# Performance work log

Measured on AMD Instinct MI355X. Metric: run time of the kernel, lower is better.

Reference implementation:

```python
import jax, jax.numpy as jnp
import numpy as np

SEQ, BATCH, EMBED = 2048, 4, 768
NUM_HEADS = 12
HEAD_DIM = EMBED // NUM_HEADS
SCALING = HEAD_DIM ** -0.5


def setup_inputs() -> dict:
    key = jax.random.key(0)
    ks = jax.random.split(key, 9)
    std = 0.02
    d = {"x": jax.random.normal(ks[0], (SEQ, BATCH, EMBED), dtype=jnp.float32)}
    for i, n in enumerate(["q", "k", "v", "out"]):
        d[f"W{n}"] = jax.random.normal(ks[1 + 2 * i], (EMBED, EMBED), dtype=jnp.float32) * std
        d[f"b{n}"] = jax.random.normal(ks[2 + 2 * i], (EMBED,), dtype=jnp.float32) * std
    return d


def reference(x, Wq, bq, Wk, bk, Wv, bv, Wout, bout):
    # x: [tgt_len, bsz, embed_dim] (fairseq seq-first layout per forward body)
    T, B, E = x.shape
    H, Dh = NUM_HEADS, HEAD_DIM

    q = (x @ Wq.T + bq) * SCALING          # [T, B, E]
    k = x @ Wk.T + bk
    v = x @ Wv.T + bv

    # view(T, B*H, Dh).transpose(0, 1) -> [B*H, T, Dh]
    q = q.reshape(T, B * H, Dh).transpose(1, 0, 2)
    k = k.reshape(T, B * H, Dh).transpose(1, 0, 2)
    v = v.reshape(T, B * H, Dh).transpose(1, 0, 2)

    # bmm: [B*H, T, T] attention scores (full O(T^2) matrix, as in the original)
    scores = jnp.einsum('bqd,bkd->bqk', q, k)
    # util_softmax with onnx_trace=True: softmax in float32, then cast back
    probs = jax.nn.softmax(scores.astype(jnp.float32), axis=-1).astype(scores.dtype)
    # dropout p=0.0 -> identity

    attn = jnp.einsum('bqk,bkd->bqd', probs, v)           # [B*H, T, Dh]
    attn = attn.transpose(1, 0, 2).reshape(T, B, E)       # [T, B, E]
    return attn @ Wout.T + bout
```

## Files before the change

kernel.cpp:

```cpp
#include <hip/hip_runtime.h>
#include <hip/hip_bf16.h>

#define SEQ 2048
#define BATCH 4
#define EMBED 768
#define NHEAD 12
#define HDIM 64
#define NROWS (SEQ*BATCH)
#define GH (BATCH*NHEAD)
#define KVBLK 64

typedef __bf16 bf16;
typedef __attribute__((ext_vector_type(4))) __bf16 bf16x4;
typedef __attribute__((ext_vector_type(8))) __bf16 bf16x8;
typedef __attribute__((ext_vector_type(4))) float f32x4;

#define LOG2E 1.44269504088896340736f

__global__ __launch_bounds__(256) void cvt_kernel(const float* __restrict__ in,
                                                  bf16* __restrict__ out, int n4) {
  int i = blockIdx.x * 256 + threadIdx.x;
  if (i >= n4) return;
  float4 v = reinterpret_cast<const float4*>(in)[i];
  bf16x4 o;
  o[0] = (bf16)v.x; o[1] = (bf16)v.y; o[2] = (bf16)v.z; o[3] = (bf16)v.w;
  reinterpret_cast<bf16x4*>(out)[i] = o;
}

__global__ __launch_bounds__(256) void cvt_w4(const float* __restrict__ Wq,
                                              const float* __restrict__ Wk,
                                              const float* __restrict__ Wv,
                                              const float* __restrict__ Wo,
                                              bf16* __restrict__ Wqkvb,
                                              bf16* __restrict__ Wob) {
  const int n4 = EMBED * EMBED / 4;
  int i = blockIdx.x * 256 + threadIdx.x;
  if (i >= n4) return;
  const float* src;
  bf16* dst;
  switch (blockIdx.y) {
    case 0: src = Wq; dst = Wqkvb; break;
    case 1: src = Wk; dst = Wqkvb + EMBED * EMBED; break;
    case 2: src = Wv; dst = Wqkvb + 2 * EMBED * EMBED; break;
    default: src = Wo; dst = Wob; break;
  }
  float4 v = reinterpret_cast<const float4*>(src)[i];
  bf16x4 o;
  o[0] = (bf16)v.x; o[1] = (bf16)v.y; o[2] = (bf16)v.z; o[3] = (bf16)v.w;
  reinterpret_cast<bf16x4*>(dst)[i] = o;
}

__global__ __launch_bounds__(256) void gemm_qkv(const bf16* __restrict__ A,
                                                const bf16* __restrict__ B,
                                                const float* __restrict__ bq,
                                                const float* __restrict__ bk,
                                                const float* __restrict__ bv,
                                                bf16* __restrict__ Qh,
                                                bf16* __restrict__ Kh,
                                                bf16* __restrict__ Vt) {
  constexpr int K = EMBED;
  __shared__ bf16 As[128 * 32];
  __shared__ bf16 Bs[128 * 32];
  const int tid = threadIdx.x;
  const int l = tid & 63;
  const int w = tid >> 6;
  const int row0 = blockIdx.x * 128;
  const int col0 = blockIdx.y * 128;
  const int wm = (w >> 1) * 64;
  const int wn = (w & 1) * 64;
  const int l15 = l & 15, l4 = l >> 4;

  f32x4 acc[4][4] = {};

  for (int k0 = 0; k0 < K; k0 += 32) {
#pragma unroll
    for (int i = 0; i < 2; ++i) {
      int c = tid + i * 256;
      int r = c >> 2, cc = c & 3;
      __builtin_amdgcn_global_load_lds(
          (const __attribute__((address_space(1))) void*)(A + (size_t)(row0 + r) * K + k0 + cc * 8),
          (__attribute__((address_space(3))) void*)(As + c * 8), 16, 0, 0);
    }
#pragma unroll
    for (int i = 0; i < 2; ++i) {
      int c = tid + i * 256;
      int r = c >> 2, cc = c & 3;
      __builtin_amdgcn_global_load_lds(
          (const __attribute__((address_space(1))) void*)(B + (size_t)(col0 + r) * K + k0 + cc * 8),
          (__attribute__((address_space(3))) void*)(Bs + c * 8), 16, 0, 0);
    }
    __syncthreads();

    bf16x8 af[4], bfr[4];
#pragma unroll
    for (int i = 0; i < 4; ++i)
      af[i] = *reinterpret_cast<const bf16x8*>(&As[(wm + i * 16 + l15) * 32 + l4 * 8]);
#pragma unroll
    for (int j = 0; j < 4; ++j)
      bfr[j] = *reinterpret_cast<const bf16x8*>(&Bs[(wn + j * 16 + l15) * 32 + l4 * 8]);
#pragma unroll
    for (int i = 0; i < 4; ++i)
#pragma unroll
      for (int j = 0; j < 4; ++j)
        acc[i][j] = __builtin_amdgcn_mfma_f32_16x16x32_bf16(af[i], bfr[j], acc[i][j], 0, 0, 0);
    __syncthreads();
  }

  const int sel = blockIdx.y / 6;
  const float* bias = sel == 0 ? bq : (sel == 1 ? bk : bv);
  const int colbase = col0 - sel * EMBED;
#pragma unroll
  for (int i = 0; i < 4; ++i) {
#pragma unroll
    for (int j = 0; j < 4; ++j) {
      int col = colbase + wn + j * 16 + l15;
      float bia = bias[col];
#pragma unroll
      for (int r = 0; r < 4; ++r) {
        int row = row0 + wm + i * 16 + l4 * 4 + r;
        float v = acc[i][j][r] + bia;
        int t = row >> 2, bb = row & 3;
        int hh = col >> 6, d = col & 63;
        int g = bb * NHEAD + hh;
        if (sel == 0)      Qh[((size_t)g * SEQ + t) * HDIM + d] = (bf16)(v * (0.125f * LOG2E));
        else if (sel == 1) Kh[((size_t)g * SEQ + t) * HDIM + d] = (bf16)v;
        else               Vt[((size_t)g * HDIM + d) * SEQ + t] = (bf16)v;
      }
    }
  }
}

__global__ __launch_bounds__(256) void gemm_out(const bf16* __restrict__ A,
                                                const bf16* __restrict__ B,
                                                const float* __restrict__ bias,
                                                float* __restrict__ outp) {
  constexpr int K = EMBED;
  __shared__ bf16 As[128 * 32];
  __shared__ bf16 Bs[128 * 32];
  const int tid = threadIdx.x;
  const int l = tid & 63;
  const int w = tid >> 6;
  const int row0 = blockIdx.x * 128;
  const int col0 = blockIdx.y * 128;
  const int wm = (w >> 1) * 64;
  const int wn = (w & 1) * 64;
  const int l15 = l & 15, l4 = l >> 4;

  f32x4 acc[4][4] = {};

  for (int k0 = 0; k0 < K; k0 += 32) {
#pragma unroll
    for (int i = 0; i < 2; ++i) {
      int c = tid + i * 256;
      int r = c >> 2, cc = c & 3;
      __builtin_amdgcn_global_load_lds(
          (const __attribute__((address_space(1))) void*)(A + (size_t)(row0 + r) * K + k0 + cc * 8),
          (__attribute__((address_space(3))) void*)(As + c * 8), 16, 0, 0);
    }
#pragma unroll
    for (int i = 0; i < 2; ++i) {
      int c = tid + i * 256;
      int r = c >> 2, cc = c & 3;
      __builtin_amdgcn_global_load_lds(
          (const __attribute__((address_space(1))) void*)(B + (size_t)(col0 + r) * K + k0 + cc * 8),
          (__attribute__((address_space(3))) void*)(Bs + c * 8), 16, 0, 0);
    }
    __syncthreads();

    bf16x8 af[4], bfr[4];
#pragma unroll
    for (int i = 0; i < 4; ++i)
      af[i] = *reinterpret_cast<const bf16x8*>(&As[(wm + i * 16 + l15) * 32 + l4 * 8]);
#pragma unroll
    for (int j = 0; j < 4; ++j)
      bfr[j] = *reinterpret_cast<const bf16x8*>(&Bs[(wn + j * 16 + l15) * 32 + l4 * 8]);
#pragma unroll
    for (int i = 0; i < 4; ++i)
#pragma unroll
      for (int j = 0; j < 4; ++j)
        acc[i][j] = __builtin_amdgcn_mfma_f32_16x16x32_bf16(af[i], bfr[j], acc[i][j], 0, 0, 0);
    __syncthreads();
  }

#pragma unroll
  for (int i = 0; i < 4; ++i) {
#pragma unroll
    for (int j = 0; j < 4; ++j) {
      int col = col0 + wn + j * 16 + l15;
      float bia = bias[col];
#pragma unroll
      for (int r = 0; r < 4; ++r) {
        int row = row0 + wm + i * 16 + l4 * 4 + r;
        outp[(size_t)row * EMBED + col] = acc[i][j][r] + bia;
      }
    }
  }
}

__global__ __launch_bounds__(256, 3) void attn_kernel(const bf16* __restrict__ Qh,
                                                      const bf16* __restrict__ Kh,
                                                      const bf16* __restrict__ Vt,
                                                      bf16* __restrict__ attnb) {
  const int g = blockIdx.x % GH;
  const int q0 = (blockIdx.x / GH) * 128;
  const int tid = threadIdx.x;
  const int w = tid >> 6, l = tid & 63;
  const int l15 = l & 15, l4 = l >> 4;
  const int qw = q0 + w * 32;

  __shared__ bf16 Ks[2][KVBLK * HDIM];
  __shared__ bf16 Vs[2][HDIM * KVBLK];
  __shared__ bf16 P_all[4][32 * 64];

  bf16* P = (bf16*)P_all[w];
  const bf16* Qp = Qh + (size_t)g * SEQ * HDIM;
  const bf16* Kp = Kh + (size_t)g * SEQ * HDIM;
  const bf16* Vp = Vt + (size_t)g * HDIM * SEQ;

#define STAGE(buf, kv0)                                                                 \
  do {                                                                                  \
    _Pragma("unroll") for (int i = 0; i < 2; ++i) {                                     \
      int t = i * 256 + tid;                                                            \
      int r = t >> 3, c = t & 7;                                                        \
      __builtin_amdgcn_global_load_lds(                                                 \
          (const __attribute__((address_space(1))) void*)(Kp + (size_t)((kv0) + r) * HDIM + ((c ^ (r & 7)) * 8)), \
          (__attribute__((address_space(3))) void*)(&Ks[buf][t * 8]), 16, 0, 0);        \
    }                                                                                   \
    _Pragma("unroll") for (int i = 0; i < 2; ++i) {                                     \
      int t = i * 256 + tid;                                                            \
      int r = t >> 3, c = t & 7;                                                        \
      __builtin_amdgcn_global_load_lds(                                                 \
          (const __attribute__((address_space(1))) void*)(Vp + (size_t)r * SEQ + (kv0) + ((c ^ (r & 7)) * 8)), \
          (__attribute__((address_space(3))) void*)(&Vs[buf][t * 8]), 16, 0, 0);        \
    }                                                                                   \
  } while (0)

  bf16x8 aq[2][2];
#pragma unroll
  for (int qf = 0; qf < 2; ++qf)
#pragma unroll
    for (int ks = 0; ks < 2; ++ks)
      aq[qf][ks] = *reinterpret_cast<const bf16x8*>(
          Qp + (size_t)(qw + qf * 16 + l15) * HDIM + ks * 32 + l4 * 8);

  f32x4 acco[2][4] = {};
  float lsum[2] = {0.f, 0.f};

  STAGE(0, 0);
  __syncthreads();

  int cur = 0;
  for (int kv0 = 0; kv0 < SEQ; kv0 += KVBLK) {
    if (kv0 + KVBLK < SEQ) STAGE(cur ^ 1, kv0 + KVBLK);

    f32x4 s[2][4] = {};
#pragma unroll
    for (int kf = 0; kf < 4; ++kf) {
      int row = kf * 16 + l15;
#pragma unroll
      for (int ks = 0; ks < 2; ++ks) {
        bf16x8 bk = *reinterpret_cast<const bf16x8*>(
            &Ks[cur][row * 64 + (((ks * 4 + l4) ^ (row & 7)) * 8)]);
        __builtin_amdgcn_s_setprio(1);
        s[0][kf] = __builtin_amdgcn_mfma_f32_16x16x32_bf16(bk, aq[0][ks], s[0][kf], 0, 0, 0);
        s[1][kf] = __builtin_amdgcn_mfma_f32_16x16x32_bf16(bk, aq[1][ks], s[1][kf], 0, 0, 0);
        __builtin_amdgcn_s_setprio(0);
      }
    }

#pragma unroll
    for (int qf = 0; qf < 2; ++qf) {
      int prow = qf * 16 + l15;
#pragma unroll
      for (int kf = 0; kf < 4; ++kf) {
        float p0 = exp2f(s[qf][kf][0]);
        float p1 = exp2f(s[qf][kf][1]);
        float p2 = exp2f(s[qf][kf][2]);
        float p3 = exp2f(s[qf][kf][3]);
        lsum[qf] += (p0 + p1) + (p2 + p3);
        bf16x4 pk;
        pk[0] = (bf16)p0; pk[1] = (bf16)p1; pk[2] = (bf16)p2; pk[3] = (bf16)p3;
        int chunk = (2 * kf + (l4 >> 1)) ^ (prow & 7);
        *reinterpret_cast<bf16x4*>(&P[prow * 64 + chunk * 8 + (l4 & 1) * 4]) = pk;
      }
    }

#pragma unroll
    for (int ks = 0; ks < 2; ++ks) {
      bf16x8 ap[2];
#pragma unroll
      for (int qf = 0; qf < 2; ++qf) {
        int prow = qf * 16 + l15;
        int lc = ks * 4 + l4;
        ap[qf] = *reinterpret_cast<const bf16x8*>(P + prow * 64 + ((lc ^ (prow & 7)) << 3));
      }
#pragma unroll
      for (int df = 0; df < 4; ++df) {
        int row = df * 16 + l15;
        bf16x8 bv = *reinterpret_cast<const bf16x8*>(
            &Vs[cur][row * 64 + (((ks * 4 + l4) ^ (row & 7)) * 8)]);
        __builtin_amdgcn_s_setprio(1);
        acco[0][df] = __builtin_amdgcn_mfma_f32_16x16x32_bf16(ap[0], bv, acco[0][df], 0, 0, 0);
        acco[1][df] = __builtin_amdgcn_mfma_f32_16x16x32_bf16(ap[1], bv, acco[1][df], 0, 0, 0);
        __builtin_amdgcn_s_setprio(0);
      }
    }
    __syncthreads();
    cur ^= 1;
  }

  float rinv[2][4];
#pragma unroll
  for (int qf = 0; qf < 2; ++qf) {
    float t = lsum[qf];
    t += __shfl_xor(t, 16);
    t += __shfl_xor(t, 32);
#pragma unroll
    for (int r = 0; r < 4; ++r) {
      int src = (l & 48) | (l4 * 4 + r);
      rinv[qf][r] = __builtin_amdgcn_rcpf(__shfl(t, src));
    }
  }

  const int bb = g / NHEAD, hh = g % NHEAD;
#pragma unroll
  for (int qf = 0; qf < 2; ++qf)
#pragma unroll
    for (int df = 0; df < 4; ++df)
#pragma unroll
      for (int r = 0; r < 4; ++r) {
        int tq = qw + qf * 16 + l4 * 4 + r;
        int d = df * 16 + l15;
        float v = acco[qf][df][r] * rinv[qf][r];
        attnb[((size_t)tq * BATCH + bb) * EMBED + hh * HDIM + d] = (bf16)v;
      }
}

extern "C" void kernel_launch(void* const* d_in, const int* in_sizes, int n_in,
                              void* d_out, int out_size, void* d_ws, size_t ws_size,
                              hipStream_t stream) {
  const float* x  = (const float*)d_in[0];
  const float* Wq = (const float*)d_in[1];
  const float* bq = (const float*)d_in[2];
  const float* Wk = (const float*)d_in[3];
  const float* bk = (const float*)d_in[4];
  const float* Wv = (const float*)d_in[5];
  const float* bv = (const float*)d_in[6];
  const float* Wo = (const float*)d_in[7];
  const float* bo = (const float*)d_in[8];
  float* out = (float*)d_out;

  char* ws = (char*)d_ws;
  bf16* xb    = (bf16*)(ws + 0);
  bf16* Wqkvb = (bf16*)(ws + 12582912);
  bf16* Wob   = (bf16*)(ws + 16121856);
  bf16* Qh    = (bf16*)(ws + 17301504);
  bf16* Kh    = (bf16*)(ws + 29884416);
  bf16* Vt    = (bf16*)(ws + 42467328);
  bf16* attnb = (bf16*)(ws + 55050240);

  cvt_kernel<<<6144, 256, 0, stream>>>(x, xb, NROWS * EMBED / 4);
  cvt_w4<<<dim3(576, 4), 256, 0, stream>>>(Wq, Wk, Wv, Wo, Wqkvb, Wob);

  gemm_qkv<<<dim3(NROWS / 128, 18), 256, 0, stream>>>(xb, Wqkvb, bq, bk, bv, Qh, Kh, Vt);

  attn_kernel<<<GH * (SEQ / 128), 256, 0, stream>>>(Qh, Kh, Vt, attnb);

  gemm_out<<<dim3(NROWS / 128, EMBED / 128), 256, 0, stream>>>(attnb, Wob, bo, out);
}
```

Baseline: 171.6 us.

## Shrink attention query tile to 64 and compute row sums via MFMA

The attention kernel now processes 16 query rows per wave (64 per block) instead of 32, doubling the grid and raising the occupancy target to 5 blocks per CU. V is single-buffered and staged each iteration, while K stays double-buffered, with an explicit vmcnt wait placed before the PV stage. P is split into two 32-column halves to cut LDS use. Row sums are now accumulated with an extra MFMA against a ones vector rather than shuffle reductions. The smaller tile halves K/V reuse per block and adds more global K/V traffic, in exchange for more parallelism, lower register and LDS pressure, and overlap of the softmax with MFMA work.

```diff
diff --git a/kernel.cpp b/kernel.cpp
--- a/kernel.cpp
+++ b/kernel.cpp
@@ -197,27 +197,27 @@
   }
 }
 
-__global__ __launch_bounds__(256, 3) void attn_kernel(const bf16* __restrict__ Qh,
+__global__ __launch_bounds__(256, 5) void attn_kernel(const bf16* __restrict__ Qh,
                                                       const bf16* __restrict__ Kh,
                                                       const bf16* __restrict__ Vt,
                                                       bf16* __restrict__ attnb) {
   const int g = blockIdx.x % GH;
-  const int q0 = (blockIdx.x / GH) * 128;
+  const int q0 = (blockIdx.x / GH) * 64;
   const int tid = threadIdx.x;
   const int w = tid >> 6, l = tid & 63;
   const int l15 = l & 15, l4 = l >> 4;
-  const int qw = q0 + w * 32;
+  const int qw = q0 + w * 16;
 
   __shared__ bf16 Ks[2][KVBLK * HDIM];
-  __shared__ bf16 Vs[2][HDIM * KVBLK];
-  __shared__ bf16 P_all[4][32 * 64];
+  __shared__ bf16 Vs[HDIM * KVBLK];
+  __shared__ bf16 P_all[4][16 * 32];
 
   bf16* P = (bf16*)P_all[w];
   const bf16* Qp = Qh + (size_t)g * SEQ * HDIM;
   const bf16* Kp = Kh + (size_t)g * SEQ * HDIM;
   const bf16* Vp = Vt + (size_t)g * HDIM * SEQ;
 
-#define STAGE(buf, kv0)                                                                 \
+#define STAGE_K(buf, kv0)                                                               \
   do {                                                                                  \
     _Pragma("unroll") for (int i = 0; i < 2; ++i) {                                     \
       int t = i * 256 + tid;                                                            \
@@ -226,34 +226,44 @@
           (const __attribute__((address_space(1))) void*)(Kp + (size_t)((kv0) + r) * HDIM + ((c ^ (r & 7)) * 8)), \
           (__attribute__((address_space(3))) void*)(&Ks[buf][t * 8]), 16, 0, 0);        \
     }                                                                                   \
+  } while (0)
+
+#define STAGE_V(kv0)                                                                    \
+  do {                                                                                  \
     _Pragma("unroll") for (int i = 0; i < 2; ++i) {                                     \
       int t = i * 256 + tid;                                                            \
       int r = t >> 3, c = t & 7;                                                        \
       __builtin_amdgcn_global_load_lds(                                                 \
           (const __attribute__((address_space(1))) void*)(Vp + (size_t)r * SEQ + (kv0) + ((c ^ (r & 7)) * 8)), \
-          (__attribute__((address_space(3))) void*)(&Vs[buf][t * 8]), 16, 0, 0);        \
+          (__attribute__((address_space(3))) void*)(&Vs[t * 8]), 16, 0, 0);             \
     }                                                                                   \
   } while (0)
 
-  bf16x8 aq[2][2];
-#pragma unroll
-  for (int qf = 0; qf < 2; ++qf)
-#pragma unroll
-    for (int ks = 0; ks < 2; ++ks)
-      aq[qf][ks] = *reinterpret_cast<const bf16x8*>(
-          Qp + (size_t)(qw + qf * 16 + l15) * HDIM + ks * 32 + l4 * 8);
-
-  f32x4 acco[2][4] = {};
-  float lsum[2] = {0.f, 0.f};
-
-  STAGE(0, 0);
+  bf16x8 aq[2];
+#pragma unroll
+  for (int ks = 0; ks < 2; ++ks)
+    aq[ks] = *reinterpret_cast<const bf16x8*>(
+        Qp + (size_t)(qw + l15) * HDIM + ks * 32 + l4 * 8);
+
+  bf16x8 vone;
+#pragma unroll
+  for (int i = 0; i < 8; ++i) vone[i] = (bf16)1.0f;
+
+  f32x4 acco[4] = {};
+  f32x4 accs = {};
+
+  const int ppr = l15 * 32;
+  const int prd = ppr + ((l4 ^ (l15 & 3)) << 3);
+
+  STAGE_K(0, 0);
   __syncthreads();
 
   int cur = 0;
   for (int kv0 = 0; kv0 < SEQ; kv0 += KVBLK) {
-    if (kv0 + KVBLK < SEQ) STAGE(cur ^ 1, kv0 + KVBLK);
-
-    f32x4 s[2][4] = {};
+    STAGE_V(kv0);
+    STAGE_K(cur ^ 1, (kv0 + KVBLK) & (SEQ - 1));
+
+    f32x4 s[4] = {};
 #pragma unroll
     for (int kf = 0; kf < 4; ++kf) {
       int row = kf * 16 + l15;
@@ -262,78 +272,77 @@
         bf16x8 bk = *reinterpret_cast<const bf16x8*>(
             &Ks[cur][row * 64 + (((ks * 4 + l4) ^ (row & 7)) * 8)]);
         __builtin_amdgcn_s_setprio(1);
-        s[0][kf] = __builtin_amdgcn_mfma_f32_16x16x32_bf16(bk, aq[0][ks], s[0][kf], 0, 0, 0);
-        s[1][kf] = __builtin_amdgcn_mfma_f32_16x16x32_bf16(bk, aq[1][ks], s[1][kf], 0, 0, 0);
+        s[kf] = __builtin_amdgcn_mfma_f32_16x16x32_bf16(bk, aq[ks], s[kf], 0, 0, 0);
         __builtin_amdgcn_s_setprio(0);
       }
     }
 
 #pragma unroll
-    for (int qf = 0; qf < 2; ++qf) {
-      int prow = qf * 16 + l15;
-#pragma unroll
-      for (int kf = 0; kf < 4; ++kf) {
-        float p0 = exp2f(s[qf][kf][0]);
-        float p1 = exp2f(s[qf][kf][1]);
-        float p2 = exp2f(s[qf][kf][2]);
-        float p3 = exp2f(s[qf][kf][3]);
-        lsum[qf] += (p0 + p1) + (p2 + p3);
-        bf16x4 pk;
-        pk[0] = (bf16)p0; pk[1] = (bf16)p1; pk[2] = (bf16)p2; pk[3] = (bf16)p3;
-        int chunk = (2 * kf + (l4 >> 1)) ^ (prow & 7);
-        *reinterpret_cast<bf16x4*>(&P[prow * 64 + chunk * 8 + (l4 & 1) * 4]) = pk;
-      }
-    }
-
-#pragma unroll
-    for (int ks = 0; ks < 2; ++ks) {
-      bf16x8 ap[2];
-#pragma unroll
-      for (int qf = 0; qf < 2; ++qf) {
-        int prow = qf * 16 + l15;
-        int lc = ks * 4 + l4;
-        ap[qf] = *reinterpret_cast<const bf16x8*>(P + prow * 64 + ((lc ^ (prow & 7)) << 3));
-      }
+    for (int kf = 0; kf < 2; ++kf) {
+      float p0 = exp2f(s[kf][0]), p1 = exp2f(s[kf][1]);
+      float p2 = exp2f(s[kf][2]), p3 = exp2f(s[kf][3]);
+      bf16x4 pk;
+      pk[0] = (bf16)p0; pk[1] = (bf16)p1; pk[2] = (bf16)p2; pk[3] = (bf16)p3;
+      int c = (kf & 1) * 2 + (l4 >> 1);
+      *reinterpret_cast<bf16x4*>(&P[ppr + ((c ^ (l15 & 3)) << 3) + (l4 & 1) * 4]) = pk;
+    }
+    asm volatile("s_waitcnt vmcnt(2)" ::: "memory");
+    {
+      bf16x8 ap = *reinterpret_cast<const bf16x8*>(&P[prd]);
 #pragma unroll
       for (int df = 0; df < 4; ++df) {
         int row = df * 16 + l15;
         bf16x8 bv = *reinterpret_cast<const bf16x8*>(
-            &Vs[cur][row * 64 + (((ks * 4 + l4) ^ (row & 7)) * 8)]);
+            &Vs[row * 64 + ((l4 ^ (row & 7)) * 8)]);
         __builtin_amdgcn_s_setprio(1);
-        acco[0][df] = __builtin_amdgcn_mfma_f32_16x16x32_bf16(ap[0], bv, acco[0][df], 0, 0, 0);
-        acco[1][df] = __builtin_amdgcn_mfma_f32_16x16x32_bf16(ap[1], bv, acco[1][df], 0, 0, 0);
+        acco[df] = __builtin_amdgcn_mfma_f32_16x16x32_bf16(ap, bv, acco[df], 0, 0, 0);
         __builtin_amdgcn_s_setprio(0);
       }
-    }
+      __builtin_amdgcn_s_setprio(1);
+      accs = __builtin_amdgcn_mfma_f32_16x16x32_bf16(ap, vone, accs, 0, 0, 0);
+      __builtin_amdgcn_s_setprio(0);
+    }
+
+#pragma unroll
+    for (int kf = 2; kf < 4; ++kf) {
+      float p0 = exp2f(s[kf][0]), p1 = exp2f(s[kf][1]);
+      float p2 = exp2f(s[kf][2]), p3 = exp2f(s[kf][3]);
+      bf16x4 pk;
+      pk[0] = (bf16)p0; pk[1] = (bf16)p1; pk[2] = (bf16)p2; pk[3] = (bf16)p3;
+      int c = (kf & 1) * 2 + (l4 >> 1);
+      *reinterpret_cast<bf16x4*>(&P[ppr + ((c ^ (l15 & 3)) << 3) + (l4 & 1) * 4]) = pk;
+    }
+    {
+      bf16x8 ap = *reinterpret_cast<const bf16x8*>(&P[prd]);
+#pragma unroll
+      for (int df = 0; df < 4; ++df) {
+        int row = df * 16 + l15;
+        bf16x8 bv = *reinterpret_cast<const bf16x8*>(
+            &Vs[row * 64 + (((4 + l4) ^ (row & 7)) * 8)]);
+        __builtin_amdgcn_s_setprio(1);
+        acco[df] = __builtin_amdgcn_mfma_f32_16x16x32_bf16(ap, bv, acco[df], 0, 0, 0);
+        __builtin_amdgcn_s_setprio(0);
+      }
+      __builtin_amdgcn_s_setprio(1);
+      accs = __builtin_amdgcn_mfma_f32_16x16x32_bf16(ap, vone, accs, 0, 0, 0);
+      __builtin_amdgcn_s_setprio(0);
+    }
+
     __syncthreads();
     cur ^= 1;
   }
 
-  float rinv[2][4];
-#pragma unroll
-  for (int qf = 0; qf < 2; ++qf) {
-    float t = lsum[qf];
-    t += __shfl_xor(t, 16);
-    t += __shfl_xor(t, 32);
-#pragma unroll
-    for (int r = 0; r < 4; ++r) {
-      int src = (l & 48) | (l4 * 4 + r);
-      rinv[qf][r] = __builtin_amdgcn_rcpf(__shfl(t, src));
-    }
-  }
-
   const int bb = g / NHEAD, hh = g % NHEAD;
 #pragma unroll
-  for (int qf = 0; qf < 2; ++qf)
-#pragma unroll
-    for (int df = 0; df < 4; ++df)
-#pragma unroll
-      for (int r = 0; r < 4; ++r) {
-        int tq = qw + qf * 16 + l4 * 4 + r;
-        int d = df * 16 + l15;
-        float v = acco[qf][df][r] * rinv[qf][r];
-        attnb[((size_t)tq * BATCH + bb) * EMBED + hh * HDIM + d] = (bf16)v;
-      }
+  for (int r = 0; r < 4; ++r) {
+    float rinv = __builtin_amdgcn_rcpf(accs[r]);
+    int tq = qw + l4 * 4 + r;
+#pragma unroll
+    for (int df = 0; df < 4; ++df) {
+      int d = df * 16 + l15;
+      attnb[((size_t)tq * BATCH + bb) * EMBED + hh * HDIM + d] = (bf16)(acco[df][r] * rinv);
+    }
+  }
 }
 
 extern "C" void kernel_launch(void* const* d_in, const int* in_sizes, int n_in,
@@ -364,7 +373,7 @@
 
   gemm_qkv<<<dim3(NROWS / 128, 18), 256, 0, stream>>>(xb, Wqkvb, bq, bk, bv, Qh, Kh, Vt);
 
-  attn_kernel<<<GH * (SEQ / 128), 256, 0, stream>>>(Qh, Kh, Vt, attnb);
+  attn_kernel<<<GH * (SEQ / 64), 256, 0, stream>>>(Qh, Kh, Vt, attnb);
 
   gemm_out<<<dim3(NROWS / 128, EMBED / 128), 256, 0, stream>>>(attnb, Wob, bo, out);
 }
```

New measurement: 192.1 us. +11.9%, slower.

## Single-buffer V tile, compute row sums via MFMA, raise attention occupancy

Applied to the files above, without the earlier changes.

The V shared-memory tile goes from double to single buffering and is loaded at the start of each iteration, overlapping the QK^T and softmax phase, with an explicit vmcnt wait before the PV MFMAs. This frees shared memory so launch bounds can rise from 3 to 4 blocks per CU. The softmax denominator is now accumulated by an extra MFMA against a vector of ones instead of scalar adds plus cross-lane shuffles. The K prefetch now always runs, using a wrapped index on the last iteration, which adds a redundant load. The row sum is computed from bf16-rounded probabilities, which slightly changes the numerics.

```diff
diff --git a/kernel.cpp b/kernel.cpp
--- a/kernel.cpp
+++ b/kernel.cpp
@@ -197,7 +197,7 @@
   }
 }
 
-__global__ __launch_bounds__(256, 3) void attn_kernel(const bf16* __restrict__ Qh,
+__global__ __launch_bounds__(256, 4) void attn_kernel(const bf16* __restrict__ Qh,
                                                       const bf16* __restrict__ Kh,
                                                       const bf16* __restrict__ Vt,
                                                       bf16* __restrict__ attnb) {
@@ -209,7 +209,7 @@
   const int qw = q0 + w * 32;
 
   __shared__ bf16 Ks[2][KVBLK * HDIM];
-  __shared__ bf16 Vs[2][HDIM * KVBLK];
+  __shared__ bf16 Vs[HDIM * KVBLK];
   __shared__ bf16 P_all[4][32 * 64];
 
   bf16* P = (bf16*)P_all[w];
@@ -217,7 +217,7 @@
   const bf16* Kp = Kh + (size_t)g * SEQ * HDIM;
   const bf16* Vp = Vt + (size_t)g * HDIM * SEQ;
 
-#define STAGE(buf, kv0)                                                                 \
+#define STAGE_K(buf, kv0)                                                               \
   do {                                                                                  \
     _Pragma("unroll") for (int i = 0; i < 2; ++i) {                                     \
       int t = i * 256 + tid;                                                            \
@@ -226,12 +226,16 @@
           (const __attribute__((address_space(1))) void*)(Kp + (size_t)((kv0) + r) * HDIM + ((c ^ (r & 7)) * 8)), \
           (__attribute__((address_space(3))) void*)(&Ks[buf][t * 8]), 16, 0, 0);        \
     }                                                                                   \
+  } while (0)
+
+#define STAGE_V(kv0)                                                                    \
+  do {                                                                                  \
     _Pragma("unroll") for (int i = 0; i < 2; ++i) {                                     \
       int t = i * 256 + tid;                                                            \
       int r = t >> 3, c = t & 7;                                                        \
       __builtin_amdgcn_global_load_lds(                                                 \
           (const __attribute__((address_space(1))) void*)(Vp + (size_t)r * SEQ + (kv0) + ((c ^ (r & 7)) * 8)), \
-          (__attribute__((address_space(3))) void*)(&Vs[buf][t * 8]), 16, 0, 0);        \
+          (__attribute__((address_space(3))) void*)(&Vs[t * 8]), 16, 0, 0);             \
     }                                                                                   \
   } while (0)
 
@@ -243,15 +247,20 @@
       aq[qf][ks] = *reinterpret_cast<const bf16x8*>(
           Qp + (size_t)(qw + qf * 16 + l15) * HDIM + ks * 32 + l4 * 8);
 
+  bf16x8 vone;
+#pragma unroll
+  for (int i = 0; i < 8; ++i) vone[i] = (bf16)1.0f;
+
   f32x4 acco[2][4] = {};
-  float lsum[2] = {0.f, 0.f};
-
-  STAGE(0, 0);
+  f32x4 accs[2] = {};
+
+  STAGE_K(0, 0);
   __syncthreads();
 
   int cur = 0;
   for (int kv0 = 0; kv0 < SEQ; kv0 += KVBLK) {
-    if (kv0 + KVBLK < SEQ) STAGE(cur ^ 1, kv0 + KVBLK);
+    STAGE_V(kv0);
+    STAGE_K(cur ^ 1, (kv0 + KVBLK) & (SEQ - 1));
 
     f32x4 s[2][4] = {};
 #pragma unroll
@@ -277,7 +286,6 @@
         float p1 = exp2f(s[qf][kf][1]);
         float p2 = exp2f(s[qf][kf][2]);
         float p3 = exp2f(s[qf][kf][3]);
-        lsum[qf] += (p0 + p1) + (p2 + p3);
         bf16x4 pk;
         pk[0] = (bf16)p0; pk[1] = (bf16)p1; pk[2] = (bf16)p2; pk[3] = (bf16)p3;
         int chunk = (2 * kf + (l4 >> 1)) ^ (prow & 7);
@@ -285,6 +293,8 @@
       }
     }
 
+    asm volatile("s_waitcnt vmcnt(2)" ::: "memory");
+
 #pragma unroll
     for (int ks = 0; ks < 2; ++ks) {
       bf16x8 ap[2];
@@ -298,42 +308,34 @@
       for (int df = 0; df < 4; ++df) {
         int row = df * 16 + l15;
         bf16x8 bv = *reinterpret_cast<const bf16x8*>(
-            &Vs[cur][row * 64 + (((ks * 4 + l4) ^ (row & 7)) * 8)]);
+            &Vs[row * 64 + (((ks * 4 + l4) ^ (row & 7)) * 8)]);
         __builtin_amdgcn_s_setprio(1);
         acco[0][df] = __builtin_amdgcn_mfma_f32_16x16x32_bf16(ap[0], bv, acco[0][df], 0, 0, 0);
         acco[1][df] = __builtin_amdgcn_mfma_f32_16x16x32_bf16(ap[1], bv, acco[1][df], 0, 0, 0);
         __builtin_amdgcn_s_setprio(0);
       }
+      __builtin_amdgcn_s_setprio(1);
+      accs[0] = __builtin_amdgcn_mfma_f32_16x16x32_bf16(ap[0], vone, accs[0], 0, 0, 0);
+      accs[1] = __builtin_amdgcn_mfma_f32_16x16x32_bf16(ap[1], vone, accs[1], 0, 0, 0);
+      __builtin_amdgcn_s_setprio(0);
     }
     __syncthreads();
     cur ^= 1;
   }
 
-  float rinv[2][4];
-#pragma unroll
-  for (int qf = 0; qf < 2; ++qf) {
-    float t = lsum[qf];
-    t += __shfl_xor(t, 16);
-    t += __shfl_xor(t, 32);
+  const int bb = g / NHEAD, hh = g % NHEAD;
+#pragma unroll
+  for (int qf = 0; qf < 2; ++qf)
 #pragma unroll
     for (int r = 0; r < 4; ++r) {
-      int src = (l & 48) | (l4 * 4 + r);
-      rinv[qf][r] = __builtin_amdgcn_rcpf(__shfl(t, src));
-    }
-  }
-
-  const int bb = g / NHEAD, hh = g % NHEAD;
-#pragma unroll
-  for (int qf = 0; qf < 2; ++qf)
-#pragma unroll
-    for (int df = 0; df < 4; ++df)
-#pragma unroll
-      for (int r = 0; r < 4; ++r) {
-        int tq = qw + qf * 16 + l4 * 4 + r;
+      float rinv = __builtin_amdgcn_rcpf(accs[qf][r]);
+      int tq = qw + qf * 16 + l4 * 4 + r;
+#pragma unroll
+      for (int df = 0; df < 4; ++df) {
         int d = df * 16 + l15;
-        float v = acco[qf][df][r] * rinv[qf][r];
-        attnb[((size_t)tq * BATCH + bb) * EMBED + hh * HDIM + d] = (bf16)v;
-      }
+        attnb[((size_t)tq * BATCH + bb) * EMBED + hh * HDIM + d] = (bf16)(acco[qf][df][r] * rinv);
+      }
+    }
 }
 
 extern "C" void kernel_launch(void* const* d_in, const int* in_sizes, int n_in,
```

Measured after the change: 168.3 us. -2.0%, faster.
